# Kernel optimization log

Measured on AMD Instinct MI355X. Metric: run time of the kernel, lower is better.

## Reference

```python
import jax, jax.numpy as jnp
import numpy as np

N_NODES = 50000
N_EDGES = 800000
NFEAT, NHID, NCLASS = 512, 256, 128
N_UV = 2048


def gcn_layer(x, adj_row, adj_col, adj_val, W, b):
    # support = x @ W ; out = A @ support (sparse COO spmm) + b
    support = x @ W                                   # [N, out]
    msgs = adj_val[:, None] * support[adj_col]        # [E, out]
    out = jax.ops.segment_sum(msgs, adj_row, num_segments=N_NODES)
    return out + b


def setup_inputs() -> dict:
    key = jax.random.key(0)
    ks = jax.random.split(key, 12)
    u = jax.random.randint(ks[0], (N_UV,), 0, N_NODES)
    v = jax.random.randint(ks[1], (N_UV,), 0, N_NODES)
    x = jax.random.normal(ks[2], (N_NODES, NFEAT), dtype=jnp.float32)
    adj_row = jnp.sort(jax.random.randint(ks[3], (N_EDGES,), 0, N_NODES))
    adj_col = jax.random.randint(ks[4], (N_EDGES,), 0, N_NODES)
    adj_val = jax.random.uniform(ks[5], (N_EDGES,), dtype=jnp.float32)
    s1 = 1.0 / np.sqrt(NHID)
    s2 = 1.0 / np.sqrt(NCLASS)
    W1 = jax.random.uniform(ks[6], (NFEAT, NHID), minval=-s1, maxval=s1, dtype=jnp.float32)
    b1 = jax.random.uniform(ks[7], (NHID,), minval=-s1, maxval=s1, dtype=jnp.float32)
    W2 = jax.random.uniform(ks[8], (NHID, NCLASS), minval=-s2, maxval=s2, dtype=jnp.float32)
    b2 = jax.random.uniform(ks[9], (NCLASS,), minval=-s2, maxval=s2, dtype=jnp.float32)
    We = jax.random.normal(ks[10], (NCLASS, NCLASS), dtype=jnp.float32) * (1.0 / np.sqrt(NCLASS))
    return {"u": u, "v": v, "x": x, "adj_row": adj_row, "adj_col": adj_col,
            "adj_val": adj_val, "W1": W1, "b1": b1, "W2": W2, "b2": b2, "We": We}


def reference(u, v, x, adj_row, adj_col, adj_val, W1, b1, W2, b2, We):
    # layer 1: GCN + ReLU (dropout is identity in eval mode)
    h = jax.nn.relu(gcn_layer(x, adj_row, adj_col, adj_val, W1, b1))
    # layer 2: GCN
    z = gcn_layer(h, adj_row, adj_col, adj_val, W2, b2)          # [N, nclass]
    # edge scoring: sigmoid(w_edge(z[u]) @ z[v].T)
    zu = z[u] @ We.T                                             # [U, nclass] (nn.Linear: x @ W.T)
    zv = z[v]                                                    # [V, nclass]
    p_uv = jax.nn.sigmoid(zu @ zv.T)                             # [U, V]
    return p_uv
```

## Files before the change

### kernel.cpp

```cpp
#include <hip/hip_runtime.h>
#include <hip/hip_bf16.h>
#include <math.h>

#define N_NODES 50000
#define N_EDGES 800000
#define NFEAT   512
#define NHID    256
#define NCLASS  128
#define N_UV    2048

typedef __bf16 bf16x8 __attribute__((ext_vector_type(8)));
typedef short  s16x8  __attribute__((ext_vector_type(8)));
typedef float  f32x4  __attribute__((ext_vector_type(4)));

__device__ __forceinline__ unsigned short bf16_rn(float f) {
  unsigned u = __float_as_uint(f);
  u += 0x7fffu + ((u >> 16) & 1u);
  return (unsigned short)(u >> 16);
}
__device__ __forceinline__ float bf16_to_f(unsigned short h) {
  return __uint_as_float(((unsigned)h) << 16);
}

#define LDSPAD 40

template <bool ASPLIT, bool BSPLIT, bool SIGMOID>
__global__ __launch_bounds__(256, 2) void gemm_mfma_split(
    const float* __restrict__ Af,
    const unsigned short* __restrict__ Ahi, const unsigned short* __restrict__ Alo,
    const float* __restrict__ BTf,
    const unsigned short* __restrict__ BThi, const unsigned short* __restrict__ BTlo,
    float* __restrict__ C, int M, int N, int K) {
  __shared__ unsigned short sAh[128 * LDSPAD];
  __shared__ unsigned short sAl[128 * LDSPAD];
  __shared__ unsigned short sBh[128 * LDSPAD];
  __shared__ unsigned short sBl[128 * LDSPAD];

  const int tid  = threadIdx.x;
  const int lane = tid & 63;
  const int wave = tid >> 6;
  const int wm   = (wave >> 1) << 6;
  const int wn   = (wave & 1) << 6;
  const int lm   = lane & 15;
  const int quad = lane >> 4;
  const int m0   = blockIdx.y * 128;
  const int n0   = blockIdx.x * 128;

  const int r32 = tid >> 3;
  const int c32 = (tid & 7) * 4;
  const int r16 = tid >> 2;
  const int c16 = (tid & 3) * 8;

  float4 pA[4]; s16x8 pAh[2], pAl[2];
  float4 pB[4]; s16x8 pBh[2], pBl[2];

  f32x4 acc[4][4];
#pragma unroll
  for (int i = 0; i < 4; ++i)
#pragma unroll
    for (int j = 0; j < 4; ++j)
#pragma unroll
      for (int r = 0; r < 4; ++r) acc[i][j][r] = 0.f;

#define LOAD_TILE(k0)                                                          \
  do {                                                                         \
    if (ASPLIT) {                                                              \
      _Pragma("unroll") for (int p = 0; p < 4; ++p) {                          \
        const int m = m0 + p * 32 + r32;                                       \
        pA[p] = make_float4(0.f, 0.f, 0.f, 0.f);                               \
        if (m < M) pA[p] = *(const float4*)&Af[(size_t)m * K + (k0) + c32];    \
      }                                                                        \
    } else {                                                                   \
      _Pragma("unroll") for (int p = 0; p < 2; ++p) {                          \
        const int m = m0 + p * 64 + r16;                                       \
        _Pragma("unroll") for (int e = 0; e < 8; ++e) { pAh[p][e] = 0; pAl[p][e] = 0; } \
        if (m < M) {                                                           \
          pAh[p] = *(const s16x8*)&Ahi[(size_t)m * K + (k0) + c16];            \
          pAl[p] = *(const s16x8*)&Alo[(size_t)m * K + (k0) + c16];            \
        }                                                                      \
      }                                                                        \
    }                                                                          \
    if (BSPLIT) {                                                              \
      _Pragma("unroll") for (int p = 0; p < 4; ++p)                            \
        pB[p] = *(const float4*)&BTf[(size_t)(n0 + p * 32 + r32) * K + (k0) + c32]; \
    } else {                                                                   \
      _Pragma("unroll") for (int p = 0; p < 2; ++p) {                          \
        pBh[p] = *(const s16x8*)&BThi[(size_t)(n0 + p * 64 + r16) * K + (k0) + c16]; \
        pBl[p] = *(const s16x8*)&BTlo[(size_t)(n0 + p * 64 + r16) * K + (k0) + c16]; \
      }                                                                        \
    }                                                                          \
  } while (0)

#define SPLIT4(v, hv, lv)                                                      \
  hv.x = bf16_rn(v.x); lv.x = bf16_rn(v.x - bf16_to_f(hv.x));                  \
  hv.y = bf16_rn(v.y); lv.y = bf16_rn(v.y - bf16_to_f(hv.y));                  \
  hv.z = bf16_rn(v.z); lv.z = bf16_rn(v.z - bf16_to_f(hv.z));                  \
  hv.w = bf16_rn(v.w); lv.w = bf16_rn(v.w - bf16_to_f(hv.w));

#define STORE_TILE()                                                           \
  do {                                                                         \
    if (ASPLIT) {                                                              \
      _Pragma("unroll") for (int p = 0; p < 4; ++p) {                          \
        ushort4 hv, lv; SPLIT4(pA[p], hv, lv);                                 \
        const int row = p * 32 + r32;                                          \
        *(ushort4*)&sAh[row * LDSPAD + c32] = hv;                              \
        *(ushort4*)&sAl[row * LDSPAD + c32] = lv;                              \
      }                                                                        \
    } else {                                                                   \
      _Pragma("unroll") for (int p = 0; p < 2; ++p) {                          \
        const int row = p * 64 + r16;                                          \
        *(s16x8*)&sAh[row * LDSPAD + c16] = pAh[p];                            \
        *(s16x8*)&sAl[row * LDSPAD + c16] = pAl[p];                            \
      }                                                                        \
    }                                                                          \
    if (BSPLIT) {                                                              \
      _Pragma("unroll") for (int p = 0; p < 4; ++p) {                          \
        ushort4 hv, lv; SPLIT4(pB[p], hv, lv);                                 \
        const int row = p * 32 + r32;                                          \
        *(ushort4*)&sBh[row * LDSPAD + c32] = hv;                              \
        *(ushort4*)&sBl[row * LDSPAD + c32] = lv;                              \
      }                                                                        \
    } else {                                                                   \
      _Pragma("unroll") for (int p = 0; p < 2; ++p) {                          \
        const int row = p * 64 + r16;                                          \
        *(s16x8*)&sBh[row * LDSPAD + c16] = pBh[p];                            \
        *(s16x8*)&sBl[row * LDSPAD + c16] = pBl[p];                            \
      }                                                                        \
    }                                                                          \
  } while (0)

  LOAD_TILE(0);

  for (int k0 = 0; k0 < K; k0 += 32) {
    if (k0) __syncthreads();
    STORE_TILE();
    __syncthreads();
    if (k0 + 32 < K) LOAD_TILE(k0 + 32);

    bf16x8 aH[4], aL[4], bH[4], bL[4];
#pragma unroll
    for (int i = 0; i < 4; ++i) {
      const int r = wm + i * 16 + lm;
      aH[i] = __builtin_bit_cast(bf16x8, *(const s16x8*)&sAh[r * LDSPAD + quad * 8]);
      aL[i] = __builtin_bit_cast(bf16x8, *(const s16x8*)&sAl[r * LDSPAD + quad * 8]);
    }
#pragma unroll
    for (int j = 0; j < 4; ++j) {
      const int r = wn + j * 16 + lm;
      bH[j] = __builtin_bit_cast(bf16x8, *(const s16x8*)&sBh[r * LDSPAD + quad * 8]);
      bL[j] = __builtin_bit_cast(bf16x8, *(const s16x8*)&sBl[r * LDSPAD + quad * 8]);
    }
#pragma unroll
    for (int i = 0; i < 4; ++i)
#pragma unroll
      for (int j = 0; j < 4; ++j) {
        acc[i][j] = __builtin_amdgcn_mfma_f32_16x16x32_bf16(aH[i], bH[j], acc[i][j], 0, 0, 0);
        acc[i][j] = __builtin_amdgcn_mfma_f32_16x16x32_bf16(aH[i], bL[j], acc[i][j], 0, 0, 0);
        acc[i][j] = __builtin_amdgcn_mfma_f32_16x16x32_bf16(aL[i], bH[j], acc[i][j], 0, 0, 0);
      }
  }

#pragma unroll
  for (int i = 0; i < 4; ++i)
#pragma unroll
    for (int j = 0; j < 4; ++j) {
      const int col = n0 + wn + j * 16 + lm;
#pragma unroll
      for (int r = 0; r < 4; ++r) {
        const int row = m0 + wm + i * 16 + quad * 4 + r;
        if (row < M) {
          float v = acc[i][j][r];
          if (SIGMOID) v = 1.f / (1.f + expf(-v));
          C[(size_t)row * N + col] = v;
        }
      }
    }
#undef LOAD_TILE
#undef STORE_TILE
#undef SPLIT4
}

__global__ __launch_bounds__(256) void split_transpose(
    const float* __restrict__ W, unsigned short* __restrict__ Thi,
    unsigned short* __restrict__ Tlo, int K, int N) {
  const int idx = blockIdx.x * 256 + threadIdx.x;
  if (idx >= K * N) return;
  const int n = idx / K;
  const int k = idx - n * K;
  const float f = W[(size_t)k * N + n];
  const unsigned short h = bf16_rn(f);
  Thi[idx] = h;
  Tlo[idx] = bf16_rn(f - bf16_to_f(h));
}

__global__ __launch_bounds__(256) void build_row_ptr(
    const int* __restrict__ rows, int* __restrict__ row_ptr) {
  const int e = blockIdx.x * 256 + threadIdx.x;
  if (e >= N_EDGES) return;
  const int r = rows[e];
  const int rprev = (e == 0) ? -1 : rows[e - 1];
  for (int n = rprev + 1; n <= r; ++n) row_ptr[n] = e;
  if (e == N_EDGES - 1) {
    for (int n = r + 1; n <= N_NODES; ++n) row_ptr[n] = N_EDGES;
  }
}

__global__ __launch_bounds__(256) void spmm256_split(
    const float4* __restrict__ S4, const int* __restrict__ row_ptr,
    const int* __restrict__ cols, const float* __restrict__ vals,
    const float4* __restrict__ bias4,
    unsigned short* __restrict__ outHi, unsigned short* __restrict__ outLo) {
  const int wave = threadIdx.x >> 6;
  const int lane = threadIdx.x & 63;
  const int node = blockIdx.x * 4 + wave;

  const int lo = row_ptr[node];
  const int hi = row_ptr[node + 1];

  float4 acc = make_float4(0.f, 0.f, 0.f, 0.f);
  int e = lo;
  for (; e + 4 <= hi; e += 4) {
    const int c0 = cols[e + 0], c1 = cols[e + 1], c2 = cols[e + 2], c3 = cols[e + 3];
    const float w0 = vals[e + 0], w1 = vals[e + 1], w2 = vals[e + 2], w3 = vals[e + 3];
    const float4 r0 = S4[(size_t)c0 * 64 + lane];
    const float4 r1 = S4[(size_t)c1 * 64 + lane];
    const float4 r2 = S4[(size_t)c2 * 64 + lane];
    const float4 r3 = S4[(size_t)c3 * 64 + lane];
    acc.x = fmaf(w0, r0.x, acc.x); acc.y = fmaf(w0, r0.y, acc.y);
    acc.z = fmaf(w0, r0.z, acc.z); acc.w = fmaf(w0, r0.w, acc.w);
    acc.x = fmaf(w1, r1.x, acc.x); acc.y = fmaf(w1, r1.y, acc.y);
    acc.z = fmaf(w1, r1.z, acc.z); acc.w = fmaf(w1, r1.w, acc.w);
    acc.x = fmaf(w2, r2.x, acc.x); acc.y = fmaf(w2, r2.y, acc.y);
    acc.z = fmaf(w2, r2.z, acc.z); acc.w = fmaf(w2, r2.w, acc.w);
    acc.x = fmaf(w3, r3.x, acc.x); acc.y = fmaf(w3, r3.y, acc.y);
    acc.z = fmaf(w3, r3.z, acc.z); acc.w = fmaf(w3, r3.w, acc.w);
  }
  for (; e < hi; ++e) {
    const int c = cols[e];
    const float w = vals[e];
    const float4 r = S4[(size_t)c * 64 + lane];
    acc.x = fmaf(w, r.x, acc.x); acc.y = fmaf(w, r.y, acc.y);
    acc.z = fmaf(w, r.z, acc.z); acc.w = fmaf(w, r.w, acc.w);
  }

  const float4 b = bias4[lane];
  acc.x = fmaxf(acc.x + b.x, 0.f);
  acc.y = fmaxf(acc.y + b.y, 0.f);
  acc.z = fmaxf(acc.z + b.z, 0.f);
  acc.w = fmaxf(acc.w + b.w, 0.f);

  ushort4 hv, lv;
  hv.x = bf16_rn(acc.x); lv.x = bf16_rn(acc.x - bf16_to_f(hv.x));
  hv.y = bf16_rn(acc.y); lv.y = bf16_rn(acc.y - bf16_to_f(hv.y));
  hv.z = bf16_rn(acc.z); lv.z = bf16_rn(acc.z - bf16_to_f(hv.z));
  hv.w = bf16_rn(acc.w); lv.w = bf16_rn(acc.w - bf16_to_f(hv.w));
  const size_t o = (size_t)node * NHID + lane * 4;
  *(ushort4*)&outHi[o] = hv;
  *(ushort4*)&outLo[o] = lv;
}

__global__ __launch_bounds__(256) void spmm128_f32(
    const float4* __restrict__ S4, const int* __restrict__ row_ptr,
    const int* __restrict__ cols, const float* __restrict__ vals,
    const float4* __restrict__ bias4, float4* __restrict__ out4) {
  const int wave = threadIdx.x >> 6;
  const int lane = threadIdx.x & 63;
  const int half = lane >> 5;
  const int l32  = lane & 31;
  const int node = blockIdx.x * 4 + wave;

  const int lo = row_ptr[node];
  const int hi = row_ptr[node + 1];

  float4 acc = make_float4(0.f, 0.f, 0.f, 0.f);
  int e = lo + half;
  for (; e + 2 < hi; e += 4) {
    const int c0 = cols[e], c1 = cols[e + 2];
    const float w0 = vals[e], w1 = vals[e + 2];
    const float4 r0 = S4[(size_t)c0 * 32 + l32];
    const float4 r1 = S4[(size_t)c1 * 32 + l32];
    acc.x = fmaf(w0, r0.x, acc.x); acc.y = fmaf(w0, r0.y, acc.y);
    acc.z = fmaf(w0, r0.z, acc.z); acc.w = fmaf(w0, r0.w, acc.w);
    acc.x = fmaf(w1, r1.x, acc.x); acc.y = fmaf(w1, r1.y, acc.y);
    acc.z = fmaf(w1, r1.z, acc.z); acc.w = fmaf(w1, r1.w, acc.w);
  }
  for (; e < hi; e += 2) {
    const int c = cols[e];
    const float w = vals[e];
    const float4 r = S4[(size_t)c * 32 + l32];
    acc.x = fmaf(w, r.x, acc.x); acc.y = fmaf(w, r.y, acc.y);
    acc.z = fmaf(w, r.z, acc.z); acc.w = fmaf(w, r.w, acc.w);
  }

  acc.x += __shfl_xor(acc.x, 32);
  acc.y += __shfl_xor(acc.y, 32);
  acc.z += __shfl_xor(acc.z, 32);
  acc.w += __shfl_xor(acc.w, 32);

  if (half == 0) {
    const float4 b = bias4[l32];
    acc.x += b.x; acc.y += b.y; acc.z += b.z; acc.w += b.w;
    out4[(size_t)node * 32 + l32] = acc;
  }
}

__global__ __launch_bounds__(128) void gather_rows(
    const float* __restrict__ Z, const int* __restrict__ idx,
    float* __restrict__ out) {
  out[blockIdx.x * NCLASS + threadIdx.x] =
      Z[(size_t)idx[blockIdx.x] * NCLASS + threadIdx.x];
}

extern "C" void kernel_launch(void* const* d_in, const int* in_sizes, int n_in,
                              void* d_out, int out_size, void* d_ws, size_t ws_size,
                              hipStream_t stream) {
  const int*   u       = (const int*)  d_in[0];
  const int*   v       = (const int*)  d_in[1];
  const float* x       = (const float*)d_in[2];
  const int*   adj_row = (const int*)  d_in[3];
  const int*   adj_col = (const int*)  d_in[4];
  const float* adj_val = (const float*)d_in[5];
  const float* W1      = (const float*)d_in[6];
  const float* b1      = (const float*)d_in[7];
  const float* W2      = (const float*)d_in[8];
  const float* b2      = (const float*)d_in[9];
  const float* We      = (const float*)d_in[10];
  float* out = (float*)d_out;

  char* wsb = (char*)d_ws;
  float* S1 = (float*)wsb;
  float* S2 = (float*)wsb;
  float* Z  = (float*)(wsb + (size_t)N_NODES * NCLASS * sizeof(float));
  char* rB = wsb + (size_t)N_NODES * NHID * sizeof(float);
  unsigned short* Hhi = (unsigned short*)rB;
  unsigned short* Hlo = Hhi + (size_t)N_NODES * NHID;
  float* ZUG = (float*)rB;
  float* ZV  = ZUG + N_UV * NCLASS;
  float* ZU  = ZV + N_UV * NCLASS;
  unsigned short* W1Thi = (unsigned short*)out;
  unsigned short* W1Tlo = W1Thi + NHID * NFEAT;
  unsigned short* W2Thi = W1Tlo + NHID * NFEAT;
  unsigned short* W2Tlo = W2Thi + NCLASS * NHID;
  int* row_ptr = (int*)(W2Tlo + NCLASS * NHID);

  split_transpose<<<(NFEAT * NHID + 255) / 256, 256, 0, stream>>>(W1, W1Thi, W1Tlo, NFEAT, NHID);
  split_transpose<<<(NHID * NCLASS + 255) / 256, 256, 0, stream>>>(W2, W2Thi, W2Tlo, NHID, NCLASS);
  build_row_ptr<<<(N_EDGES + 255) / 256, 256, 0, stream>>>(adj_row, row_ptr);

  gemm_mfma_split<true, false, false><<<dim3(NHID / 128, (N_NODES + 127) / 128), 256, 0, stream>>>(
      x, nullptr, nullptr, nullptr, W1Thi, W1Tlo, S1, N_NODES, NHID, NFEAT);

  spmm256_split<<<N_NODES / 4, 256, 0, stream>>>(
      (const float4*)S1, row_ptr, adj_col, adj_val, (const float4*)b1, Hhi, Hlo);

  gemm_mfma_split<false, false, false><<<dim3(NCLASS / 128, (N_NODES + 127) / 128), 256, 0, stream>>>(
      nullptr, Hhi, Hlo, nullptr, W2Thi, W2Tlo, S2, N_NODES, NCLASS, NHID);

  spmm128_f32<<<N_NODES / 4, 256, 0, stream>>>(
      (const float4*)S2, row_ptr, adj_col, adj_val, (const float4*)b2, (float4*)Z);

  gather_rows<<<N_UV, NCLASS, 0, stream>>>(Z, u, ZUG);
  gather_rows<<<N_UV, NCLASS, 0, stream>>>(Z, v, ZV);

  gemm_mfma_split<true, true, false><<<dim3(NCLASS / 128, N_UV / 128), 256, 0, stream>>>(
      ZUG, nullptr, nullptr, We, nullptr, nullptr, ZU, N_UV, NCLASS, NCLASS);

  gemm_mfma_split<true, true, true><<<dim3(N_UV / 128, N_UV / 128), 256, 0, stream>>>(
      ZU, nullptr, nullptr, ZV, nullptr, nullptr, out, N_UV, N_UV, NCLASS);
}
```

Before: 429.7 us.

## Fuse prep kernels, fold row gathers into GEMM loads, deepen SpMM unrolling

Merges the weight split-transpose and row_ptr build into one prep kernel. Removes the gather_rows kernels by giving the GEMM indexed A/B row loads, so the two small edge-scoring GEMMs read Z rows through u and v directly. Widens the SpMM inner loops to issue 8 or 4 independent row loads per iteration, giving more memory-level parallelism. Each gathered row load now needs an extra index lookup, and the unrolled loops use more registers.

```diff
diff --git a/kernel.cpp b/kernel.cpp
--- a/kernel.cpp
+++ b/kernel.cpp
@@ -9,9 +9,9 @@
 #define NCLASS  128
 #define N_UV    2048
 
-typedef __bf16 bf16x8 __attribute__((ext_vector_type(8)));
-typedef short  s16x8  __attribute__((ext_vector_type(8)));
-typedef float  f32x4  __attribute__((ext_vector_type(4)));
+typedef __bf16    bf16x8 __attribute__((ext_vector_type(8)));
+typedef short     s16x8  __attribute__((ext_vector_type(8)));
+typedef float     f32x4  __attribute__((ext_vector_type(4)));
 
 __device__ __forceinline__ unsigned short bf16_rn(float f) {
   unsigned u = __float_as_uint(f);
@@ -24,12 +24,14 @@
 
 #define LDSPAD 40
 
-template <bool ASPLIT, bool BSPLIT, bool SIGMOID>
+template <bool ASPLIT, bool BSPLIT, bool SIGMOID, bool AIDX, bool BIDX>
 __global__ __launch_bounds__(256, 2) void gemm_mfma_split(
     const float* __restrict__ Af,
     const unsigned short* __restrict__ Ahi, const unsigned short* __restrict__ Alo,
+    const int* __restrict__ Aidx,
     const float* __restrict__ BTf,
     const unsigned short* __restrict__ BThi, const unsigned short* __restrict__ BTlo,
+    const int* __restrict__ Bidx,
     float* __restrict__ C, int M, int N, int K) {
   __shared__ unsigned short sAh[128 * LDSPAD];
   __shared__ unsigned short sAl[128 * LDSPAD];
@@ -68,7 +70,10 @@
       _Pragma("unroll") for (int p = 0; p < 4; ++p) {                          \
         const int m = m0 + p * 32 + r32;                                       \
         pA[p] = make_float4(0.f, 0.f, 0.f, 0.f);                               \
-        if (m < M) pA[p] = *(const float4*)&Af[(size_t)m * K + (k0) + c32];    \
+        if (m < M) {                                                           \
+          const int ra = AIDX ? Aidx[m] : m;                                   \
+          pA[p] = *(const float4*)&Af[(size_t)ra * K + (k0) + c32];            \
+        }                                                                      \
       }                                                                        \
     } else {                                                                   \
       _Pragma("unroll") for (int p = 0; p < 2; ++p) {                          \
@@ -81,8 +86,11 @@
       }                                                                        \
     }                                                                          \
     if (BSPLIT) {                                                              \
-      _Pragma("unroll") for (int p = 0; p < 4; ++p)                            \
-        pB[p] = *(const float4*)&BTf[(size_t)(n0 + p * 32 + r32) * K + (k0) + c32]; \
+      _Pragma("unroll") for (int p = 0; p < 4; ++p) {                          \
+        const int n = n0 + p * 32 + r32;                                       \
+        const int rb = BIDX ? Bidx[n] : n;                                     \
+        pB[p] = *(const float4*)&BTf[(size_t)rb * K + (k0) + c32];             \
+      }                                                                        \
     } else {                                                                   \
       _Pragma("unroll") for (int p = 0; p < 2; ++p) {                          \
         pBh[p] = *(const s16x8*)&BThi[(size_t)(n0 + p * 64 + r16) * K + (k0) + c16]; \
@@ -180,28 +188,35 @@
 #undef SPLIT4
 }
 
-__global__ __launch_bounds__(256) void split_transpose(
-    const float* __restrict__ W, unsigned short* __restrict__ Thi,
-    unsigned short* __restrict__ Tlo, int K, int N) {
+__global__ __launch_bounds__(256) void prep_all(
+    const int* __restrict__ rows, int* __restrict__ row_ptr,
+    const float* __restrict__ W1, unsigned short* __restrict__ W1Thi,
+    unsigned short* __restrict__ W1Tlo,
+    const float* __restrict__ W2, unsigned short* __restrict__ W2Thi,
+    unsigned short* __restrict__ W2Tlo) {
   const int idx = blockIdx.x * 256 + threadIdx.x;
-  if (idx >= K * N) return;
-  const int n = idx / K;
-  const int k = idx - n * K;
-  const float f = W[(size_t)k * N + n];
-  const unsigned short h = bf16_rn(f);
-  Thi[idx] = h;
-  Tlo[idx] = bf16_rn(f - bf16_to_f(h));
-}
-
-__global__ __launch_bounds__(256) void build_row_ptr(
-    const int* __restrict__ rows, int* __restrict__ row_ptr) {
-  const int e = blockIdx.x * 256 + threadIdx.x;
-  if (e >= N_EDGES) return;
-  const int r = rows[e];
-  const int rprev = (e == 0) ? -1 : rows[e - 1];
-  for (int n = rprev + 1; n <= r; ++n) row_ptr[n] = e;
-  if (e == N_EDGES - 1) {
-    for (int n = r + 1; n <= N_NODES; ++n) row_ptr[n] = N_EDGES;
+  if (idx < N_EDGES) {
+    const int r = rows[idx];
+    const int rprev = (idx == 0) ? -1 : rows[idx - 1];
+    for (int n = rprev + 1; n <= r; ++n) row_ptr[n] = idx;
+    if (idx == N_EDGES - 1)
+      for (int n = r + 1; n <= N_NODES; ++n) row_ptr[n] = N_EDGES;
+  }
+  if (idx < NFEAT * NHID) {
+    const int n = idx / NFEAT;
+    const int k = idx - n * NFEAT;
+    const float f = W1[(size_t)k * NHID + n];
+    const unsigned short h = bf16_rn(f);
+    W1Thi[idx] = h;
+    W1Tlo[idx] = bf16_rn(f - bf16_to_f(h));
+  }
+  if (idx < NHID * NCLASS) {
+    const int n = idx / NHID;
+    const int k = idx - n * NHID;
+    const float f = W2[(size_t)k * NCLASS + n];
+    const unsigned short h = bf16_rn(f);
+    W2Thi[idx] = h;
+    W2Tlo[idx] = bf16_rn(f - bf16_to_f(h));
   }
 }
 
@@ -219,21 +234,18 @@
 
   float4 acc = make_float4(0.f, 0.f, 0.f, 0.f);
   int e = lo;
-  for (; e + 4 <= hi; e += 4) {
-    const int c0 = cols[e + 0], c1 = cols[e + 1], c2 = cols[e + 2], c3 = cols[e + 3];
-    const float w0 = vals[e + 0], w1 = vals[e + 1], w2 = vals[e + 2], w3 = vals[e + 3];
-    const float4 r0 = S4[(size_t)c0 * 64 + lane];
-    const float4 r1 = S4[(size_t)c1 * 64 + lane];
-    const float4 r2 = S4[(size_t)c2 * 64 + lane];
-    const float4 r3 = S4[(size_t)c3 * 64 + lane];
-    acc.x = fmaf(w0, r0.x, acc.x); acc.y = fmaf(w0, r0.y, acc.y);
-    acc.z = fmaf(w0, r0.z, acc.z); acc.w = fmaf(w0, r0.w, acc.w);
-    acc.x = fmaf(w1, r1.x, acc.x); acc.y = fmaf(w1, r1.y, acc.y);
-    acc.z = fmaf(w1, r1.z, acc.z); acc.w = fmaf(w1, r1.w, acc.w);
-    acc.x = fmaf(w2, r2.x, acc.x); acc.y = fmaf(w2, r2.y, acc.y);
-    acc.z = fmaf(w2, r2.z, acc.z); acc.w = fmaf(w2, r2.w, acc.w);
-    acc.x = fmaf(w3, r3.x, acc.x); acc.y = fmaf(w3, r3.y, acc.y);
-    acc.z = fmaf(w3, r3.z, acc.z); acc.w = fmaf(w3, r3.w, acc.w);
+  for (; e + 8 <= hi; e += 8) {
+    int c[8]; float w[8];
+#pragma unroll
+    for (int t = 0; t < 8; ++t) { c[t] = cols[e + t]; w[t] = vals[e + t]; }
+    float4 r[8];
+#pragma unroll
+    for (int t = 0; t < 8; ++t) r[t] = S4[(size_t)c[t] * 64 + lane];
+#pragma unroll
+    for (int t = 0; t < 8; ++t) {
+      acc.x = fmaf(w[t], r[t].x, acc.x); acc.y = fmaf(w[t], r[t].y, acc.y);
+      acc.z = fmaf(w[t], r[t].z, acc.z); acc.w = fmaf(w[t], r[t].w, acc.w);
+    }
   }
   for (; e < hi; ++e) {
     const int c = cols[e];
@@ -274,15 +286,18 @@
 
   float4 acc = make_float4(0.f, 0.f, 0.f, 0.f);
   int e = lo + half;
-  for (; e + 2 < hi; e += 4) {
-    const int c0 = cols[e], c1 = cols[e + 2];
-    const float w0 = vals[e], w1 = vals[e + 2];
-    const float4 r0 = S4[(size_t)c0 * 32 + l32];
-    const float4 r1 = S4[(size_t)c1 * 32 + l32];
-    acc.x = fmaf(w0, r0.x, acc.x); acc.y = fmaf(w0, r0.y, acc.y);
-    acc.z = fmaf(w0, r0.z, acc.z); acc.w = fmaf(w0, r0.w, acc.w);
-    acc.x = fmaf(w1, r1.x, acc.x); acc.y = fmaf(w1, r1.y, acc.y);
-    acc.z = fmaf(w1, r1.z, acc.z); acc.w = fmaf(w1, r1.w, acc.w);
+  for (; e + 6 < hi; e += 8) {
+    int c[4]; float w[4];
+#pragma unroll
+    for (int t = 0; t < 4; ++t) { c[t] = cols[e + 2 * t]; w[t] = vals[e + 2 * t]; }
+    float4 r[4];
+#pragma unroll
+    for (int t = 0; t < 4; ++t) r[t] = S4[(size_t)c[t] * 32 + l32];
+#pragma unroll
+    for (int t = 0; t < 4; ++t) {
+      acc.x = fmaf(w[t], r[t].x, acc.x); acc.y = fmaf(w[t], r[t].y, acc.y);
+      acc.z = fmaf(w[t], r[t].z, acc.z); acc.w = fmaf(w[t], r[t].w, acc.w);
+    }
   }
   for (; e < hi; e += 2) {
     const int c = cols[e];
@@ -302,13 +317,6 @@
     acc.x += b.x; acc.y += b.y; acc.z += b.z; acc.w += b.w;
     out4[(size_t)node * 32 + l32] = acc;
   }
-}
-
-__global__ __launch_bounds__(128) void gather_rows(
-    const float* __restrict__ Z, const int* __restrict__ idx,
-    float* __restrict__ out) {
-  out[blockIdx.x * NCLASS + threadIdx.x] =
-      Z[(size_t)idx[blockIdx.x] * NCLASS + threadIdx.x];
 }
 
 extern "C" void kernel_launch(void* const* d_in, const int* in_sizes, int n_in,
@@ -334,37 +342,39 @@
   char* rB = wsb + (size_t)N_NODES * NHID * sizeof(float);
   unsigned short* Hhi = (unsigned short*)rB;
   unsigned short* Hlo = Hhi + (size_t)N_NODES * NHID;
-  float* ZUG = (float*)rB;
-  float* ZV  = ZUG + N_UV * NCLASS;
-  float* ZU  = ZV + N_UV * NCLASS;
+  float* ZU = (float*)rB;
   unsigned short* W1Thi = (unsigned short*)out;
   unsigned short* W1Tlo = W1Thi + NHID * NFEAT;
   unsigned short* W2Thi = W1Tlo + NHID * NFEAT;
   unsigned short* W2Tlo = W2Thi + NCLASS * NHID;
   int* row_ptr = (int*)(W2Tlo + NCLASS * NHID);
 
-  split_transpose<<<(NFEAT * NHID + 255) / 256, 256, 0, stream>>>(W1, W1Thi, W1Tlo, NFEAT, NHID);
-  split_transpose<<<(NHID * NCLASS + 255) / 256, 256, 0, stream>>>(W2, W2Thi, W2Tlo, NHID, NCLASS);
-  build_row_ptr<<<(N_EDGES + 255) / 256, 256, 0, stream>>>(adj_row, row_ptr);
-
-  gemm_mfma_split<true, false, false><<<dim3(NHID / 128, (N_NODES + 127) / 128), 256, 0, stream>>>(
-      x, nullptr, nullptr, nullptr, W1Thi, W1Tlo, S1, N_NODES, NHID, NFEAT);
+  prep_all<<<(N_EDGES + 255) / 256, 256, 0, stream>>>(
+      adj_row, row_ptr, W1, W1Thi, W1Tlo, W2, W2Thi, W2Tlo);
+
+  gemm_mfma_split<true, false, false, false, false>
+      <<<dim3(NHID / 128, (N_NODES + 127) / 128), 256, 0, stream>>>(
+      x, nullptr, nullptr, nullptr, nullptr, W1Thi, W1Tlo, nullptr,
+      S1, N_NODES, NHID, NFEAT);
 
   spmm256_split<<<N_NODES / 4, 256, 0, stream>>>(
       (const float4*)S1, row_ptr, adj_col, adj_val, (const float4*)b1, Hhi, Hlo);
 
-  gemm_mfma_split<false, false, false><<<dim3(NCLASS / 128, (N_NODES + 127) / 128), 256, 0, stream>>>(
-      nullptr, Hhi, Hlo, nullptr, W2Thi, W2Tlo, S2, N_NODES, NCLASS, NHID);
+  gemm_mfma_split<false, false, false, false, false>
+      <<<dim3(NCLASS / 128, (N_NODES + 127) / 128), 256, 0, stream>>>(
+      nullptr, Hhi, Hlo, nullptr, nullptr, W2Thi, W2Tlo, nullptr,
+      S2, N_NODES, NCLASS, NHID);
 
   spmm128_f32<<<N_NODES / 4, 256, 0, stream>>>(
       (const float4*)S2, row_ptr, adj_col, adj_val, (const float4*)b2, (float4*)Z);
 
-  gather_rows<<<N_UV, NCLASS, 0, stream>>>(Z, u, ZUG);
-  gather_rows<<<N_UV, NCLASS, 0, stream>>>(Z, v, ZV);
-
-  gemm_mfma_split<true, true, false><<<dim3(NCLASS / 128, N_UV / 128), 256, 0, stream>>>(
-      ZUG, nullptr, nullptr, We, nullptr, nullptr, ZU, N_UV, NCLASS, NCLASS);
-
-  gemm_mfma_split<true, true, true><<<dim3(N_UV / 128, N_UV / 128), 256, 0, stream>>>(
-      ZU, nullptr, nullptr, ZV, nullptr, nullptr, out, N_UV, N_UV, NCLASS);
-}
+  gemm_mfma_split<true, true, false, true, false>
+      <<<dim3(NCLASS / 128, N_UV / 128), 256, 0, stream>>>(
+      Z, nullptr, nullptr, u, We, nullptr, nullptr, nullptr,
+      ZU, N_UV, NCLASS, NCLASS);
+
+  gemm_mfma_split<true, true, true, false, true>
+      <<<dim3(N_UV / 128, N_UV / 128), 256, 0, stream>>>(
+      ZU, nullptr, nullptr, nullptr, Z, nullptr, nullptr, v,
+      out, N_UV, N_UV, NCLASS);
+}
```

Result: no change. 422.0 us (-1.8%).
